# Optimization experiments

Hardware: AMD Instinct MI355X
Metric: run time of the kernel (lower is better)

## Reference

```python
import jax, jax.numpy as jnp
import numpy as np

B, N_ATOM, N_TOK = 1, 1536, 384
C_ATOM, C_PAIR, C_TOK = 128, 16, 384
C_HID, H, L = 32, 4, 3
HID = 2 * C_ATOM  # n_transition = 2
N_QUERY, N_KEY, INF = 32, 128, 1e9


def _ln(x, gamma=None, beta=None, eps=1e-5):
    mu = jnp.mean(x, axis=-1, keepdims=True)
    var = jnp.mean(jnp.square(x - mu), axis=-1, keepdims=True)
    y = (x - mu) * jax.lax.rsqrt(var + eps)
    if gamma is not None:
        y = y * gamma
    if beta is not None:
        y = y + beta
    return y


def _adaln(a, s, gamma_s, Wg, bg, Ws):
    an = _ln(a)            # LN without affine
    sn = _ln(s, gamma_s)   # scale-only LN
    return jax.nn.sigmoid(sn @ Wg + bg) * an + sn @ Ws


def _block_mask():
    # AtomTransformer.forward: 32-query x 128-key block-local mask
    offset = N_QUERY // 2 - 0.5
    n_center = N_ATOM // N_QUERY + 1
    centers = offset + jnp.arange(n_center, dtype=jnp.float32) * N_QUERY
    idx = jnp.arange(N_ATOM, dtype=jnp.float32)[:, None]
    row = (jnp.abs(idx - centers[None, :]) < N_QUERY / 2).astype(jnp.float32)
    col = (jnp.abs(idx - centers[None, :]) < N_KEY / 2).astype(jnp.float32)
    return (row @ col.T - 1.0) * INF   # [N,N]: 0 in-window, -INF outside


def _forward(ref_pos, ref_mask, ref_element, ref_charge, ref_atom_name_chars,
             ref_space_uid, token_mask, atom_to_token_index,
             W_feats, W_ref_offset, W_inv_sq, W_valid, W_l, W_m,
             W_mlp1, W_mlp2, W_mlp3, W_out_tok,
             attn_ada_gamma_s, attn_ada_Wg, attn_ada_bg, attn_ada_Ws,
             Wq, bq, Wk, Wv, lnz_g, lnz_b, Wb, Wgate, Wo, Wsg, bsg,
             tr_ada_gamma_s, tr_ada_Wg, tr_ada_bg, tr_ada_Ws,
             tr_W1, tr_W2, tr_Wog, tr_bog, tr_Wout):
    # --- RefAtomFeatureEmbedder (AF3 Alg 5 lines 1-6) ---
    feats = jnp.concatenate([
        ref_pos, ref_mask[..., None], ref_element, ref_charge[..., None],
        ref_atom_name_chars.reshape(B, N_ATOM, -1), ref_space_uid[..., None]], axis=-1)
    cl = feats @ W_feats                                     # [B,N,C_ATOM]
    d = ref_pos[:, None, :, :] - ref_pos[:, :, None, :]      # d[l,m] = pos[m]-pos[l]
    v = (ref_space_uid[:, None, :] == ref_space_uid[:, :, None]).astype(jnp.float32)[..., None]
    plm = (d @ W_ref_offset) * v
    inv_sq = 1.0 / (1.0 + jnp.sum(d * d, axis=-1, keepdims=True))
    plm = plm + (inv_sq @ W_inv_sq) * v + (v @ W_valid) * v  # [B,N,N,C_PAIR]
    ql = cl
    # --- single -> pair conditioning + pair MLP ---
    crelu = jax.nn.relu(cl)
    plm = plm + (crelu @ W_l)[:, :, None, :] + (crelu @ W_m)[:, None, :, :]
    h = jax.nn.relu(plm) @ W_mlp1
    h = jax.nn.relu(h) @ W_mlp2
    h = jax.nn.relu(h) @ W_mlp3
    plm = plm + h
    # --- AtomTransformer (Alg 7) -> DiffusionTransformer (Alg 23) ---
    beta = _block_mask()                                     # [N,N]
    atom_mask = jnp.einsum('blt,bt->bl', atom_to_token_index, token_mask)
    mask_bias = (atom_mask - 1.0)[:, None, None, :] * INF    # [B,1,1,N]
    a, s = ql, cl
    inv_sqrt = 1.0 / np.sqrt(C_HID)
    for i in range(L):
        # AttentionPairBias (Alg 24)
        an = _adaln(a, s, attn_ada_gamma_s[i], attn_ada_Wg[i], attn_ada_bg[i], attn_ada_Ws[i])
        q = (an @ Wq[i] + bq[i]).reshape(B, N_ATOM, H, C_HID)
        k = (an @ Wk[i]).reshape(B, N_ATOM, H, C_HID)
        vv = (an @ Wv[i]).reshape(B, N_ATOM, H, C_HID)
        zb = _ln(plm, lnz_g[i], lnz_b[i]) @ Wb[i]            # [B,N,N,H]
        logits = (jnp.einsum('bqhc,bkhc->bhqk', q, k) * inv_sqrt
                  + jnp.moveaxis(zb, -1, 1) + beta[None, None] + mask_bias)
        A = jax.nn.softmax(logits, axis=-1)
        o = jnp.einsum('bhqk,bkhc->bqhc', A, vv)
        g = jax.nn.sigmoid(an @ Wgate[i]).reshape(B, N_ATOM, H, C_HID)
        o = (g * o).reshape(B, N_ATOM, H * C_HID) @ Wo[i]
        attn_out = jax.nn.sigmoid(s @ Wsg[i] + bsg[i]) * o
        # ConditionedTransitionBlock (Alg 25) on pre-attention a (Alg 23)
        tn = _adaln(a, s, tr_ada_gamma_s[i], tr_ada_Wg[i], tr_ada_bg[i], tr_ada_Ws[i])
        hh = jax.nn.silu(tn @ tr_W1[i]) * (tn @ tr_W2[i])
        tr_out = jax.nn.sigmoid(s @ tr_Wog[i] + tr_bog[i]) * (hh @ tr_Wout[i])
        a = attn_out + tr_out
    # --- mean-aggregate atoms -> tokens (Alg 5 line 15) ---
    al = jax.nn.relu(a @ W_out_tok)                          # [B,N,C_TOK]
    counts = jnp.maximum(jnp.sum(atom_to_token_index, axis=1), 1.0)
    a_tok = jnp.einsum('blt,blc->btc', atom_to_token_index, al) / counts[..., None]
    return a_tok


def setup_inputs() -> dict:
    key = jax.random.key(0)
    ks = iter(jax.random.split(key, 80))

    def nrm(shape, scale=0.02):
        return jax.random.normal(next(ks), shape, dtype=jnp.float32) * scale

    inp = {}
    inp['ref_pos'] = jax.random.normal(next(ks), (B, N_ATOM, 3), dtype=jnp.float32) * 3.0
    inp['ref_mask'] = jnp.ones((B, N_ATOM), jnp.float32)
    elem = jax.random.randint(next(ks), (B, N_ATOM), 0, 128)
    inp['ref_element'] = jax.nn.one_hot(elem, 128, dtype=jnp.float32)
    inp['ref_charge'] = jax.random.normal(next(ks), (B, N_ATOM), dtype=jnp.float32)
    chars = jax.random.randint(next(ks), (B, N_ATOM, 4), 0, 64)
    inp['ref_atom_name_chars'] = jax.nn.one_hot(chars, 64, dtype=jnp.float32)
    inp['ref_space_uid'] = jnp.broadcast_to(
        (jnp.arange(N_ATOM) // 8).astype(jnp.float32), (B, N_ATOM))
    inp['token_mask'] = jnp.ones((B, N_TOK), jnp.float32)
    tok = (jnp.arange(N_ATOM) * N_TOK) // N_ATOM  # ~4 atoms per token
    inp['atom_to_token_index'] = jnp.broadcast_to(
        jax.nn.one_hot(tok, N_TOK, dtype=jnp.float32), (B, N_ATOM, N_TOK))
    # embedder params
    inp['W_feats'] = nrm((390, C_ATOM))
    inp['W_ref_offset'] = nrm((3, C_PAIR))
    inp['W_inv_sq'] = nrm((1, C_PAIR))
    inp['W_valid'] = nrm((1, C_PAIR))
    inp['W_l'] = nrm((C_ATOM, C_PAIR))
    inp['W_m'] = nrm((C_ATOM, C_PAIR))
    inp['W_mlp1'] = nrm((C_PAIR, C_PAIR))
    inp['W_mlp2'] = nrm((C_PAIR, C_PAIR))
    inp['W_mlp3'] = nrm((C_PAIR, C_PAIR))
    inp['W_out_tok'] = nrm((C_ATOM, C_TOK))
    # DiffusionTransformer params, stacked over L blocks
    inp['attn_ada_gamma_s'] = jnp.ones((L, C_ATOM), jnp.float32)
    inp['attn_ada_Wg'] = nrm((L, C_ATOM, C_ATOM))
    inp['attn_ada_bg'] = jnp.zeros((L, C_ATOM), jnp.float32)
    inp['attn_ada_Ws'] = nrm((L, C_ATOM, C_ATOM))
    inp['Wq'] = nrm((L, C_ATOM, H * C_HID))
    inp['bq'] = jnp.zeros((L, H * C_HID), jnp.float32)
    inp['Wk'] = nrm((L, C_ATOM, H * C_HID))
    inp['Wv'] = nrm((L, C_ATOM, H * C_HID))
    inp['lnz_g'] = jnp.ones((L, C_PAIR), jnp.float32)
    inp['lnz_b'] = jnp.zeros((L, C_PAIR), jnp.float32)
    inp['Wb'] = nrm((L, C_PAIR, H))
    inp['Wgate'] = nrm((L, C_ATOM, H * C_HID))
    inp['Wo'] = nrm((L, H * C_HID, C_ATOM))
    inp['Wsg'] = nrm((L, C_ATOM, C_ATOM))
    inp['bsg'] = jnp.full((L, C_ATOM), -2.0, jnp.float32)
    inp['tr_ada_gamma_s'] = jnp.ones((L, C_ATOM), jnp.float32)
    inp['tr_ada_Wg'] = nrm((L, C_ATOM, C_ATOM))
    inp['tr_ada_bg'] = jnp.zeros((L, C_ATOM), jnp.float32)
    inp['tr_ada_Ws'] = nrm((L, C_ATOM, C_ATOM))
    inp['tr_W1'] = nrm((L, C_ATOM, HID))
    inp['tr_W2'] = nrm((L, C_ATOM, HID))
    inp['tr_Wog'] = nrm((L, C_ATOM, C_ATOM))
    inp['tr_bog'] = jnp.full((L, C_ATOM), -2.0, jnp.float32)
    inp['tr_Wout'] = nrm((L, HID, C_ATOM))
    return inp


def reference(ref_pos, ref_mask, ref_element, ref_charge, ref_atom_name_chars,
              ref_space_uid, token_mask, atom_to_token_index,
              W_feats, W_ref_offset, W_inv_sq, W_valid, W_l, W_m,
              W_mlp1, W_mlp2, W_mlp3, W_out_tok,
              attn_ada_gamma_s, attn_ada_Wg, attn_ada_bg, attn_ada_Ws,
              Wq, bq, Wk, Wv, lnz_g, lnz_b, Wb, Wgate, Wo, Wsg, bsg,
              tr_ada_gamma_s, tr_ada_Wg, tr_ada_bg, tr_ada_Ws,
              tr_W1, tr_W2, tr_Wog, tr_bog, tr_Wout):
    return _forward(ref_pos, ref_mask, ref_element, ref_charge, ref_atom_name_chars,
                    ref_space_uid, token_mask, atom_to_token_index,
                    W_feats, W_ref_offset, W_inv_sq, W_valid, W_l, W_m,
                    W_mlp1, W_mlp2, W_mlp3, W_out_tok,
                    attn_ada_gamma_s, attn_ada_Wg, attn_ada_bg, attn_ada_Ws,
                    Wq, bq, Wk, Wv, lnz_g, lnz_b, Wb, Wgate, Wo, Wsg, bsg,
                    tr_ada_gamma_s, tr_ada_Wg, tr_ada_bg, tr_ada_Ws,
                    tr_W1, tr_W2, tr_Wog, tr_bog, tr_Wout)
```

## Files before the change

kernel.cpp:

```cpp
#include <hip/hip_runtime.h>
#include <math.h>

#define N_ATOM 1536
#define NB     48
#define NLAYER 3
#define NC     196608L
#define ZSTRIDE 786432L

struct GD { const float* A; const float* B; float* C; const float* ks; const float* bias;
            int act; int ldb; int ldc; int _pad; };
struct GB { GD g[18]; };

__global__ __launch_bounds__(128) void embed_tok_kernel(
    const float* __restrict__ pos, const float* __restrict__ rmask,
    const float* __restrict__ elem, const float* __restrict__ charge,
    const float* __restrict__ chars, const float* __restrict__ uid,
    const float* __restrict__ Wf, const float* __restrict__ W_l, const float* __restrict__ W_m,
    const float* __restrict__ a2t, const float* __restrict__ tmask,
    float* __restrict__ cl, float* __restrict__ aa, float* __restrict__ clnorm,
    float* __restrict__ pl, float* __restrict__ pm,
    int* __restrict__ tok, float* __restrict__ counts, float* __restrict__ amask)
{
  int l = blockIdx.x, c = threadIdx.x;
  __shared__ int sidx[6];
  __shared__ float red[128];
  __shared__ float crow[128];
  if (elem[(long)l * 128 + c] > 0.5f) sidx[0] = c;
  float v0 = chars[(long)l * 256 + c];
  if (v0 > 0.5f) sidx[1 + (c >> 6)] = c & 63;
  float v1 = chars[(long)l * 256 + 128 + c];
  if (v1 > 0.5f) sidx[3 + (c >> 6)] = c & 63;
  for (int j = c; j < 384; j += 128)
    if (a2t[(long)l * 384 + j] > 0.5f) sidx[5] = j;
  __syncthreads();
  float acc = pos[l * 3 + 0] * Wf[c]
            + pos[l * 3 + 1] * Wf[128 + c]
            + pos[l * 3 + 2] * Wf[256 + c]
            + rmask[l] * Wf[384 + c]
            + Wf[(4 + sidx[0]) * 128 + c]
            + charge[l] * Wf[132 * 128 + c]
            + Wf[(133 + sidx[1]) * 128 + c]
            + Wf[(197 + sidx[2]) * 128 + c]
            + Wf[(261 + sidx[3]) * 128 + c]
            + Wf[(325 + sidx[4]) * 128 + c]
            + uid[l] * Wf[389 * 128 + c];
  long gi = (long)l * 128 + c;
  cl[gi] = acc; aa[gi] = acc; crow[c] = fmaxf(acc, 0.f);
  red[c] = acc; __syncthreads();
  for (int s = 64; s > 0; s >>= 1) { if (c < s) red[c] += red[c + s]; __syncthreads(); }
  float mu = red[0] * (1.f / 128.f); __syncthreads();
  float d = acc - mu; red[c] = d * d; __syncthreads();
  for (int s = 64; s > 0; s >>= 1) { if (c < s) red[c] += red[c + s]; __syncthreads(); }
  clnorm[gi] = d * rsqrtf(red[0] * (1.f / 128.f) + 1e-5f);
  if (c < 32) {
    const float* W = (c < 16) ? W_l : W_m;
    int o = c & 15;
    float s = 0.f;
    for (int cc = 0; cc < 128; cc++) s = fmaf(crow[cc], W[cc * 16 + o], s);
    if (c < 16) pl[l * 16 + o] = s; else pm[l * 16 + o] = s;
  }
  if (c == 127) {
    int j = sidx[5];
    tok[l] = j; amask[l] = tmask[j];
    atomicAdd(counts + j, 1.0f);
  }
}

__global__ __launch_bounds__(128) void adaln_kernel(
    const float* __restrict__ a,
    const float* __restrict__ sgA, const float* __restrict__ adA,
    const float* __restrict__ sgT, const float* __restrict__ adT,
    float* __restrict__ an, float* __restrict__ tn)
{
  __shared__ float red[128];
  int l = blockIdx.x, c = threadIdx.x;
  float x = a[(long)l * 128 + c];
  red[c] = x; __syncthreads();
  for (int s = 64; s > 0; s >>= 1) { if (c < s) red[c] += red[c + s]; __syncthreads(); }
  float mu = red[0] * (1.f / 128.f); __syncthreads();
  float d = x - mu; red[c] = d * d; __syncthreads();
  for (int s = 64; s > 0; s >>= 1) { if (c < s) red[c] += red[c + s]; __syncthreads(); }
  float nv = d * rsqrtf(red[0] * (1.f / 128.f) + 1e-5f);
  long i = (long)l * 128 + c;
  an[i] = sgA[i] * nv + adA[i];
  tn[i] = sgT[i] * nv + adT[i];
}

__device__ __forceinline__ void gemm64_body(float* sm, const float* A, const float* B, float* C,
                                            const float* ks, const float* bias, int act,
                                            int ldb, int ldc, int row0, int col0) {
  float* As = sm; float* Bs = sm + 2176;
  int tid = threadIdx.x;
  int tx = tid & 15, ty = tid >> 4;
  float acc[4][4] = {};
  for (int k0 = 0; k0 < 128; k0 += 32) {
    __syncthreads();
    { int r = tid >> 3, k4 = tid & 7;
#pragma unroll
      for (int half = 0; half < 2; half++) {
        int row = r + half * 32;
        float4 v = *(const float4*)(A + (long)(row0 + row) * 128 + k0 + k4 * 4);
        if (ks) { const float* kp = ks + k0 + k4 * 4; v.x *= kp[0]; v.y *= kp[1]; v.z *= kp[2]; v.w *= kp[3]; }
        As[(k4 * 4 + 0) * 68 + row] = v.x; As[(k4 * 4 + 1) * 68 + row] = v.y;
        As[(k4 * 4 + 2) * 68 + row] = v.z; As[(k4 * 4 + 3) * 68 + row] = v.w;
      } }
    { int kk = tid >> 4, n4 = tid & 15;
#pragma unroll
      for (int half = 0; half < 2; half++) {
        int k = kk + half * 16;
        *(float4*)&Bs[k * 68 + n4 * 4] = *(const float4*)(B + (long)(k0 + k) * ldb + col0 + n4 * 4);
      } }
    __syncthreads();
#pragma unroll
    for (int kk = 0; kk < 32; kk++) {
      float4 a = *(const float4*)&As[kk * 68 + ty * 4];
      float4 b = *(const float4*)&Bs[kk * 68 + tx * 4];
      float av[4] = {a.x, a.y, a.z, a.w}, bv[4] = {b.x, b.y, b.z, b.w};
#pragma unroll
      for (int i = 0; i < 4; i++)
#pragma unroll
        for (int j = 0; j < 4; j++) acc[i][j] = fmaf(av[i], bv[j], acc[i][j]);
    }
  }
  __syncthreads();
#pragma unroll
  for (int i = 0; i < 4; i++) {
    int row = row0 + ty * 4 + i;
#pragma unroll
    for (int j = 0; j < 4; j++) {
      int col = col0 + tx * 4 + j;
      float x = acc[i][j];
      if (bias) x += bias[col];
      if (act == 1) x = 1.f / (1.f + expf(-x));
      else if (act == 2) x = fmaxf(x, 0.f);
      C[(long)row * ldc + col] = x;
    }
  }
}

__global__ __launch_bounds__(256) void gemm64(GB args, int M)
{
  __shared__ float sm[4352];
  GD d = args.g[blockIdx.z];
  gemm64_body(sm, d.A, d.B, d.C, d.ks, d.bias, d.act, d.ldb, d.ldc, blockIdx.y * 64, blockIdx.x * 64);
}

__global__ __launch_bounds__(256) void zpre_kernel(
    const float* __restrict__ pos, const float* __restrict__ uid,
    const float* __restrict__ Wro, const float* __restrict__ Winv, const float* __restrict__ Wval,
    const float* __restrict__ M1, const float* __restrict__ M2, const float* __restrict__ M3,
    const float* __restrict__ Lg, const float* __restrict__ Lb, const float* __restrict__ Wb,
    const float* __restrict__ pl, const float* __restrict__ pm, float* __restrict__ zb,
    GB ba)
{
  __shared__ float sm[4352];
  int bid = blockIdx.x, tid = threadIdx.x;
  if (bid >= 768) {
    int u = bid - 768;
    GD d = ba.g[u / 48];
    int tt = u % 48;
    gemm64_body(sm, d.A, d.B, d.C, d.ks, d.bias, d.act, d.ldb, d.ldc, (tt >> 1) * 64, (tt & 1) * 64);
    return;
  }
  if (tid < 48)  sm[tid] = Wro[tid];
  if (tid < 16)  { sm[48 + tid] = Winv[tid]; sm[64 + tid] = Wval[tid]; }
  sm[80 + tid] = M1[tid]; sm[336 + tid] = M2[tid]; sm[592 + tid] = M3[tid];
  if (tid < 48)  { sm[848 + tid] = Lg[tid]; sm[896 + tid] = Lb[tid]; }
  if (tid < 192) sm[944 + tid] = Wb[tid];
  __syncthreads();
  const float* sWro = sm;      const float* sWinv = sm + 48;  const float* sWval = sm + 64;
  const float* sM1 = sm + 80;  const float* sM2 = sm + 336;   const float* sM3 = sm + 592;
  const float* sLg = sm + 848; const float* sLb = sm + 896;   const float* sWb = sm + 944;
  int b = bid >> 4;
  int pc = (bid & 15) * 256 + tid;
  int qi = pc >> 7, kj = pc & 127;
  int l = b * 32 + qi, m = b * 32 - 48 + kj;
  long base = ((long)(b * 32 + qi) * 128 + kj) * 4;
  if (m < 0 || m >= N_ATOM) {
    for (int i = 0; i < NLAYER; i++)
      for (int h = 0; h < 4; h++) zb[i * ZSTRIDE + base + h] = 0.f;
    return;
  }
  float dx = pos[m * 3 + 0] - pos[l * 3 + 0];
  float dy = pos[m * 3 + 1] - pos[l * 3 + 1];
  float dz = pos[m * 3 + 2] - pos[l * 3 + 2];
  float v = (uid[m] == uid[l]) ? 1.f : 0.f;
  float inv = 1.f / (1.f + dx * dx + dy * dy + dz * dz);
  float pv[16], ha[16], hb[16];
#pragma unroll
  for (int j = 0; j < 16; j++)
    pv[j] = v * (dx * sWro[j] + dy * sWro[16 + j] + dz * sWro[32 + j] + inv * sWinv[j] + sWval[j])
            + pl[l * 16 + j] + pm[m * 16 + j];
#pragma unroll
  for (int jo = 0; jo < 16; jo++) { float s = 0.f; for (int ji = 0; ji < 16; ji++) s = fmaf(fmaxf(pv[ji], 0.f), sM1[ji * 16 + jo], s); ha[jo] = s; }
#pragma unroll
  for (int jo = 0; jo < 16; jo++) { float s = 0.f; for (int ji = 0; ji < 16; ji++) s = fmaf(fmaxf(ha[ji], 0.f), sM2[ji * 16 + jo], s); hb[jo] = s; }
#pragma unroll
  for (int jo = 0; jo < 16; jo++) { float s = 0.f; for (int ji = 0; ji < 16; ji++) s = fmaf(fmaxf(hb[ji], 0.f), sM3[ji * 16 + jo], s); ha[jo] = s; }
#pragma unroll
  for (int j = 0; j < 16; j++) pv[j] += ha[j];
  for (int i = 0; i < NLAYER; i++) {
    float mu = 0.f;
#pragma unroll
    for (int j = 0; j < 16; j++) mu += pv[j];
    mu *= (1.f / 16.f);
    float var = 0.f;
#pragma unroll
    for (int j = 0; j < 16; j++) { float dd = pv[j] - mu; var += dd * dd; }
    var *= (1.f / 16.f);
    float rs = rsqrtf(var + 1e-5f);
    float zn[16];
#pragma unroll
    for (int j = 0; j < 16; j++) zn[j] = (pv[j] - mu) * rs * sLg[i * 16 + j] + sLb[i * 16 + j];
    for (int h = 0; h < 4; h++) {
      float s = 0.f;
#pragma unroll
      for (int j = 0; j < 16; j++) s = fmaf(zn[j], sWb[i * 64 + j * 4 + h], s);
      zb[i * ZSTRIDE + base + h] = s;
    }
  }
}

__global__ __launch_bounds__(256) void attn_kernel(
    const float* __restrict__ qb, const float* __restrict__ kb, const float* __restrict__ vb,
    const float* __restrict__ gb, const float* __restrict__ zb, const float* __restrict__ amask,
    float* __restrict__ go)
{
  __shared__ float qs[32][36], ks[128][36], vs[128][36], ps[32][132];
  __shared__ float red[32][8];
  int b = blockIdx.x, h = blockIdx.y, t = threadIdx.x;
  int kbase = b * 32 - 48;
  {
    int qi = t >> 3, c4 = t & 7;
    *(float4*)&qs[qi][c4 * 4] = *(const float4*)(qb + (long)(b * 32 + qi) * 128 + h * 32 + c4 * 4);
  }
  for (int idx = t; idx < 128 * 8; idx += 256) {
    int kj = idx >> 3, c4 = idx & 7;
    int m = kbase + kj;
    float4 kv = make_float4(0.f, 0.f, 0.f, 0.f), vv = make_float4(0.f, 0.f, 0.f, 0.f);
    if (m >= 0 && m < N_ATOM) {
      kv = *(const float4*)(kb + (long)m * 128 + h * 32 + c4 * 4);
      vv = *(const float4*)(vb + (long)m * 128 + h * 32 + c4 * 4);
    }
    *(float4*)&ks[kj][c4 * 4] = kv;
    *(float4*)&vs[kj][c4 * 4] = vv;
  }
  __syncthreads();
  const float isq = 0.17677669529663687f;
  for (int p = t; p < 4096; p += 256) {
    int qi = p >> 7, kj = p & 127;
    int m = kbase + kj;
    float s = 0.f;
#pragma unroll
    for (int c4 = 0; c4 < 8; c4++) {
      float4 a = *(const float4*)&qs[qi][c4 * 4];
      float4 k4 = *(const float4*)&ks[kj][c4 * 4];
      s = fmaf(a.x, k4.x, s); s = fmaf(a.y, k4.y, s);
      s = fmaf(a.z, k4.z, s); s = fmaf(a.w, k4.w, s);
    }
    float logit;
    if (m >= 0 && m < N_ATOM) {
      logit = s * isq + zb[(((long)(b * 32 + qi)) * 128 + kj) * 4 + h] + (amask[m] - 1.f) * 1e9f;
    } else {
      logit = -1e9f;
    }
    ps[qi][kj] = logit;
  }
  __syncthreads();
  int row = t >> 3, ln8 = t & 7;
  float mx = -1e30f;
  for (int kj = ln8; kj < 128; kj += 8) mx = fmaxf(mx, ps[row][kj]);
  red[row][ln8] = mx; __syncthreads();
  if (ln8 == 0) {
    float m2 = red[row][0];
#pragma unroll
    for (int j = 1; j < 8; j++) m2 = fmaxf(m2, red[row][j]);
    red[row][0] = m2;
  }
  __syncthreads();
  mx = red[row][0];
  float sm = 0.f;
  for (int kj = ln8; kj < 128; kj += 8) { float e = expf(ps[row][kj] - mx); ps[row][kj] = e; sm += e; }
  __syncthreads();
  red[row][ln8] = sm; __syncthreads();
  if (ln8 == 0) {
    float s2 = 0.f;
#pragma unroll
    for (int j = 0; j < 8; j++) s2 += red[row][j];
    red[row][0] = 1.f / s2;
  }
  __syncthreads();
  float r = red[row][0];
  for (int kj = ln8; kj < 128; kj += 8) ps[row][kj] *= r;
  __syncthreads();
  {
    int qi = t >> 3, c4 = t & 7;
    float4 acc = make_float4(0.f, 0.f, 0.f, 0.f);
#pragma unroll 4
    for (int kj = 0; kj < 128; kj++) {
      float p = ps[qi][kj];
      float4 v = *(const float4*)&vs[kj][c4 * 4];
      acc.x = fmaf(p, v.x, acc.x); acc.y = fmaf(p, v.y, acc.y);
      acc.z = fmaf(p, v.z, acc.z); acc.w = fmaf(p, v.w, acc.w);
    }
    long gi = (long)(b * 32 + qi) * 128 + h * 32 + c4 * 4;
    float4 g = *(const float4*)(gb + gi);
    acc.x *= g.x; acc.y *= g.y; acc.z *= g.z; acc.w *= g.w;
    *(float4*)(go + gi) = acc;
  }
}

__global__ __launch_bounds__(256) void gemm_dual32(
    const float* __restrict__ A1, const float* __restrict__ B1,
    const float* __restrict__ h1, const float* __restrict__ h2, const float* __restrict__ B2,
    const float* __restrict__ g1, const float* __restrict__ g2,
    float* __restrict__ C)
{
  __shared__ float As[32 * 36];
  __shared__ float Bs[32 * 68];
  const int N = 128;
  int t = threadIdx.x;
  int row0 = blockIdx.y * 32, col0 = blockIdx.x * 64;
  int tx = t & 15, ty = t >> 4;
  float acc1[2][4] = {}, acc2[2][4] = {};
  for (int k0 = 0; k0 < 128; k0 += 32) {
    __syncthreads();
    { int r = t >> 3, k4 = t & 7;
      float4 v = *(const float4*)(A1 + (long)(row0 + r) * 128 + k0 + k4 * 4);
      As[(k4 * 4 + 0) * 36 + r] = v.x; As[(k4 * 4 + 1) * 36 + r] = v.y;
      As[(k4 * 4 + 2) * 36 + r] = v.z; As[(k4 * 4 + 3) * 36 + r] = v.w;
    }
    for (int e = t; e < 512; e += 256) {
      int k = e >> 4, n4 = e & 15;
      *(float4*)&Bs[k * 68 + n4 * 4] = *(const float4*)(B1 + (long)(k0 + k) * N + col0 + n4 * 4);
    }
    __syncthreads();
#pragma unroll
    for (int kk = 0; kk < 32; kk++) {
      float a0 = As[kk * 36 + ty * 2], a1 = As[kk * 36 + ty * 2 + 1];
      float4 b = *(const float4*)&Bs[kk * 68 + tx * 4];
      float bv[4] = {b.x, b.y, b.z, b.w};
#pragma unroll
      for (int j = 0; j < 4; j++) {
        acc1[0][j] = fmaf(a0, bv[j], acc1[0][j]);
        acc1[1][j] = fmaf(a1, bv[j], acc1[1][j]);
      }
    }
  }
  for (int k0 = 0; k0 < 256; k0 += 32) {
    __syncthreads();
    { int r = t >> 3, k4 = t & 7;
      long o = (long)(row0 + r) * 256 + k0 + k4 * 4;
      float4 x = *(const float4*)(h1 + o);
      float4 y = *(const float4*)(h2 + o);
      As[(k4 * 4 + 0) * 36 + r] = (x.x / (1.f + expf(-x.x))) * y.x;
      As[(k4 * 4 + 1) * 36 + r] = (x.y / (1.f + expf(-x.y))) * y.y;
      As[(k4 * 4 + 2) * 36 + r] = (x.z / (1.f + expf(-x.z))) * y.z;
      As[(k4 * 4 + 3) * 36 + r] = (x.w / (1.f + expf(-x.w))) * y.w;
    }
    for (int e = t; e < 512; e += 256) {
      int k = e >> 4, n4 = e & 15;
      *(float4*)&Bs[k * 68 + n4 * 4] = *(const float4*)(B2 + (long)(k0 + k) * N + col0 + n4 * 4);
    }
    __syncthreads();
#pragma unroll
    for (int kk = 0; kk < 32; kk++) {
      float a0 = As[kk * 36 + ty * 2], a1 = As[kk * 36 + ty * 2 + 1];
      float4 b = *(const float4*)&Bs[kk * 68 + tx * 4];
      float bv[4] = {b.x, b.y, b.z, b.w};
#pragma unroll
      for (int j = 0; j < 4; j++) {
        acc2[0][j] = fmaf(a0, bv[j], acc2[0][j]);
        acc2[1][j] = fmaf(a1, bv[j], acc2[1][j]);
      }
    }
  }
#pragma unroll
  for (int i = 0; i < 2; i++) {
    long o = (long)(row0 + ty * 2 + i) * N + col0 + tx * 4;
    float4 ga = *(const float4*)(g1 + o);
    float4 gb = *(const float4*)(g2 + o);
    float4 r;
    r.x = ga.x * acc1[i][0] + gb.x * acc2[i][0];
    r.y = ga.y * acc1[i][1] + gb.y * acc2[i][1];
    r.z = ga.z * acc1[i][2] + gb.z * acc2[i][2];
    r.w = ga.w * acc1[i][3] + gb.w * acc2[i][3];
    *(float4*)(C + o) = r;
  }
}

__global__ __launch_bounds__(256) void gemm_scatter(
    const float* __restrict__ A, const float* __restrict__ B,
    const int* __restrict__ tok, const float* __restrict__ counts,
    float* __restrict__ out, int K)
{
  __shared__ float As[32][68];
  __shared__ float Bs[32][68];
  int tid = threadIdx.x;
  int row0 = blockIdx.y * 64, col0 = blockIdx.x * 64;
  int tx = tid & 15, ty = tid >> 4;
  float acc[4][4] = {};
  for (int k0 = 0; k0 < K; k0 += 32) {
    __syncthreads();
    { int r = tid >> 3, k4 = tid & 7;
#pragma unroll
      for (int half = 0; half < 2; half++) {
        int row = r + half * 32;
        float4 v = *(const float4*)(A + (long)(row0 + row) * K + k0 + k4 * 4);
        As[k4 * 4 + 0][row] = v.x; As[k4 * 4 + 1][row] = v.y;
        As[k4 * 4 + 2][row] = v.z; As[k4 * 4 + 3][row] = v.w;
      } }
    { int kk = tid >> 4, n4 = tid & 15;
#pragma unroll
      for (int half = 0; half < 2; half++) {
        int k = kk + half * 16;
        float4 v = *(const float4*)(B + (long)(k0 + k) * 384 + col0 + n4 * 4);
        *(float4*)&Bs[k][n4 * 4] = v;
      } }
    __syncthreads();
#pragma unroll
    for (int kk = 0; kk < 32; kk++) {
      float4 a = *(const float4*)&As[kk][ty * 4];
      float4 b = *(const float4*)&Bs[kk][tx * 4];
      float av[4] = {a.x, a.y, a.z, a.w}, bv[4] = {b.x, b.y, b.z, b.w};
#pragma unroll
      for (int i = 0; i < 4; i++)
#pragma unroll
        for (int j = 0; j < 4; j++) acc[i][j] = fmaf(av[i], bv[j], acc[i][j]);
    }
  }
  __syncthreads();
#pragma unroll
  for (int i = 0; i < 4; i++) {
    int row = row0 + ty * 4 + i;
    int tk = tok[row];
    float inv = 1.f / fmaxf(counts[tk], 1.f);
#pragma unroll
    for (int j = 0; j < 4; j++) {
      int col = col0 + tx * 4 + j;
      atomicAdd(&out[(long)tk * 384 + col], fmaxf(acc[i][j], 0.f) * inv);
    }
  }
}

extern "C" void kernel_launch(void* const* d_in, const int* in_sizes, int n_in,
                              void* d_out, int out_size, void* d_ws, size_t ws_size,
                              hipStream_t stream)
{
  const float* pos    = (const float*)d_in[0];
  const float* rmask  = (const float*)d_in[1];
  const float* elem   = (const float*)d_in[2];
  const float* charge = (const float*)d_in[3];
  const float* chars  = (const float*)d_in[4];
  const float* uid    = (const float*)d_in[5];
  const float* tmask  = (const float*)d_in[6];
  const float* a2t    = (const float*)d_in[7];
  const float* Wf     = (const float*)d_in[8];
  const float* Wro    = (const float*)d_in[9];
  const float* Winv   = (const float*)d_in[10];
  const float* Wval   = (const float*)d_in[11];
  const float* W_l    = (const float*)d_in[12];
  const float* W_m    = (const float*)d_in[13];
  const float* M1     = (const float*)d_in[14];
  const float* M2     = (const float*)d_in[15];
  const float* M3     = (const float*)d_in[16];
  const float* Wtok   = (const float*)d_in[17];
  const float* gA     = (const float*)d_in[18];
  const float* WgA    = (const float*)d_in[19];
  const float* bgA    = (const float*)d_in[20];
  const float* WsA    = (const float*)d_in[21];
  const float* Wq     = (const float*)d_in[22];
  const float* bq     = (const float*)d_in[23];
  const float* Wk     = (const float*)d_in[24];
  const float* Wv     = (const float*)d_in[25];
  const float* Lg     = (const float*)d_in[26];
  const float* Lb     = (const float*)d_in[27];
  const float* Wb     = (const float*)d_in[28];
  const float* Wgate  = (const float*)d_in[29];
  const float* Wo     = (const float*)d_in[30];
  const float* Wsg    = (const float*)d_in[31];
  const float* bsg    = (const float*)d_in[32];
  const float* gT     = (const float*)d_in[33];
  const float* WgT    = (const float*)d_in[34];
  const float* bgT    = (const float*)d_in[35];
  const float* WsT    = (const float*)d_in[36];
  const float* trW1   = (const float*)d_in[37];
  const float* trW2   = (const float*)d_in[38];
  const float* Wog    = (const float*)d_in[39];
  const float* bog    = (const float*)d_in[40];
  const float* Wout   = (const float*)d_in[41];
  float* out = (float*)d_out;

  float* ws = (float*)d_ws;
  size_t off = 0;
  auto alloc = [&](size_t n) { float* p = ws + off; off += n; return p; };
  float* cl     = alloc(NC);
  float* aa     = alloc(NC);
  float* clnorm = alloc(NC);
  float* an     = alloc(NC);
  float* tn     = alloc(NC);
  float* qbuf   = alloc(NC);
  float* kbuf   = alloc(NC);
  float* vbuf   = alloc(NC);
  float* gbuf   = alloc(NC);
  float* gobuf  = alloc(NC);
  float* h1     = alloc((size_t)N_ATOM * 256);
  float* h2     = alloc((size_t)N_ATOM * 256);
  float* pl     = alloc((size_t)N_ATOM * 16);
  float* pm     = alloc((size_t)N_ATOM * 16);
  float* zbias  = alloc((size_t)NLAYER * ZSTRIDE);
  float* sgA    = alloc(NC * NLAYER);
  float* adA    = alloc(NC * NLAYER);
  float* sgT    = alloc(NC * NLAYER);
  float* adT    = alloc(NC * NLAYER);
  float* gsg    = alloc(NC * NLAYER);
  float* gog    = alloc(NC * NLAYER);
  float* counts = alloc(384);
  float* amask  = alloc(N_ATOM);
  int*   tok    = (int*)alloc(N_ATOM);
  (void)ws_size; (void)in_sizes; (void)n_in; (void)out_size;

  (void)hipMemsetAsync(counts, 0, 384 * sizeof(float), stream);
  (void)hipMemsetAsync(out, 0, (size_t)384 * 384 * sizeof(float), stream);

  embed_tok_kernel<<<N_ATOM, 128, 0, stream>>>(pos, rmask, elem, charge, chars, uid, Wf,
                                               W_l, W_m, a2t, tmask,
                                               cl, aa, clnorm, pl, pm, tok, counts, amask);

  {
    GB ba = {};
    for (int i = 0; i < NLAYER; i++) {
      size_t o = (size_t)i * NC;
      ba.g[i * 6 + 0] = { clnorm, WgA + i * 16384, sgA + o, gA + i * 128, bgA + i * 128, 1, 128, 128, 0 };
      ba.g[i * 6 + 1] = { clnorm, WsA + i * 16384, adA + o, gA + i * 128, nullptr,       0, 128, 128, 0 };
      ba.g[i * 6 + 2] = { clnorm, WgT + i * 16384, sgT + o, gT + i * 128, bgT + i * 128, 1, 128, 128, 0 };
      ba.g[i * 6 + 3] = { clnorm, WsT + i * 16384, adT + o, gT + i * 128, nullptr,       0, 128, 128, 0 };
      ba.g[i * 6 + 4] = { cl,     Wsg + i * 16384, gsg + o, nullptr,      bsg + i * 128, 1, 128, 128, 0 };
      ba.g[i * 6 + 5] = { cl,     Wog + i * 16384, gog + o, nullptr,      bog + i * 128, 1, 128, 128, 0 };
    }
    zpre_kernel<<<768 + 864, 256, 0, stream>>>(pos, uid, Wro, Winv, Wval, M1, M2, M3,
                                               Lg, Lb, Wb, pl, pm, zbias, ba);
  }

  for (int i = 0; i < NLAYER; i++) {
    size_t o = (size_t)i * NC;
    adaln_kernel<<<N_ATOM, 128, 0, stream>>>(aa, sgA + o, adA + o, sgT + o, adT + o, an, tn);
    {
      GB ba = {};
      ba.g[0] = { an, Wq + i * 16384,        qbuf, nullptr, bq + i * 128, 0, 128, 128, 0 };
      ba.g[1] = { an, Wk + i * 16384,        kbuf, nullptr, nullptr,      0, 128, 128, 0 };
      ba.g[2] = { an, Wv + i * 16384,        vbuf, nullptr, nullptr,      0, 128, 128, 0 };
      ba.g[3] = { an, Wgate + i * 16384,     gbuf, nullptr, nullptr,      1, 128, 128, 0 };
      ba.g[4] = { tn, trW1 + i * 32768,       h1,  nullptr, nullptr,      0, 256, 256, 0 };
      ba.g[5] = { tn, trW1 + i * 32768 + 128, h1 + 128, nullptr, nullptr, 0, 256, 256, 0 };
      ba.g[6] = { tn, trW2 + i * 32768,       h2,  nullptr, nullptr,      0, 256, 256, 0 };
      ba.g[7] = { tn, trW2 + i * 32768 + 128, h2 + 128, nullptr, nullptr, 0, 256, 256, 0 };
      gemm64<<<dim3(2, 24, 8), 256, 0, stream>>>(ba, N_ATOM);
    }
    attn_kernel<<<dim3(NB, 4), 256, 0, stream>>>(qbuf, kbuf, vbuf, gbuf,
                                                 zbias + (size_t)i * ZSTRIDE, amask, gobuf);
    gemm_dual32<<<dim3(2, 48), 256, 0, stream>>>(gobuf, Wo + i * 16384, h1, h2, Wout + i * 32768,
                                                 gsg + o, gog + o, aa);
  }

  gemm_scatter<<<dim3(6, 24), 256, 0, stream>>>(aa, Wtok, tok, counts, out, 128);
}
```

Before: 357.0 us.

## Fuse AdaLN into per-layer QKV/transition GEMM and precompute SwiGLU product

Removes the separate adaln kernel and its an/tn intermediate buffers. The per-layer projection GEMM now computes LayerNorm statistics and the AdaLN modulation on its A tile in shared memory. The transition blocks compute both W1 and W2 tiles at once and write silu(h1)*h2 into a single hh buffer, so gemm_dual32 reads half as much data. This cuts one launch and several global round-trips per layer, at the cost of recomputing LN per column tile and using more shared memory per block (about 52KB), which may lower occupancy.

```diff
diff --git a/kernel.cpp b/kernel.cpp
--- a/kernel.cpp
+++ b/kernel.cpp
@@ -66,26 +66,6 @@
   }
 }
 
-__global__ __launch_bounds__(128) void adaln_kernel(
-    const float* __restrict__ a,
-    const float* __restrict__ sgA, const float* __restrict__ adA,
-    const float* __restrict__ sgT, const float* __restrict__ adT,
-    float* __restrict__ an, float* __restrict__ tn)
-{
-  __shared__ float red[128];
-  int l = blockIdx.x, c = threadIdx.x;
-  float x = a[(long)l * 128 + c];
-  red[c] = x; __syncthreads();
-  for (int s = 64; s > 0; s >>= 1) { if (c < s) red[c] += red[c + s]; __syncthreads(); }
-  float mu = red[0] * (1.f / 128.f); __syncthreads();
-  float d = x - mu; red[c] = d * d; __syncthreads();
-  for (int s = 64; s > 0; s >>= 1) { if (c < s) red[c] += red[c + s]; __syncthreads(); }
-  float nv = d * rsqrtf(red[0] * (1.f / 128.f) + 1e-5f);
-  long i = (long)l * 128 + c;
-  an[i] = sgA[i] * nv + adA[i];
-  tn[i] = sgT[i] * nv + adT[i];
-}
-
 __device__ __forceinline__ void gemm64_body(float* sm, const float* A, const float* B, float* C,
                                             const float* ks, const float* bias, int act,
                                             int ldb, int ldc, int row0, int col0) {
@@ -136,13 +116,6 @@
       C[(long)row * ldc + col] = x;
     }
   }
-}
-
-__global__ __launch_bounds__(256) void gemm64(GB args, int M)
-{
-  __shared__ float sm[4352];
-  GD d = args.g[blockIdx.z];
-  gemm64_body(sm, d.A, d.B, d.C, d.ks, d.bias, d.act, d.ldb, d.ldc, blockIdx.y * 64, blockIdx.x * 64);
 }
 
 __global__ __launch_bounds__(256) void zpre_kernel(
@@ -221,6 +194,134 @@
   }
 }
 
+__global__ __launch_bounds__(256) void adaqkv_kernel(
+    const float* __restrict__ aa,
+    const float* __restrict__ sgA, const float* __restrict__ adA,
+    const float* __restrict__ sgT, const float* __restrict__ adT,
+    const float* __restrict__ Wq, const float* __restrict__ bq,
+    const float* __restrict__ Wk, const float* __restrict__ Wv, const float* __restrict__ Wgate,
+    const float* __restrict__ W1, const float* __restrict__ W2,
+    float* __restrict__ qbuf, float* __restrict__ kbuf, float* __restrict__ vbuf,
+    float* __restrict__ gbuf, float* __restrict__ hh)
+{
+  __shared__ float sm[13184];
+  float* mu = sm; float* rs = sm + 64;
+  float* Af = sm + 128; float* Bs = sm + 8832; float* B2s = sm + 11008;
+  int u = blockIdx.x, t = threadIdx.x;
+  bool tr = (u >= 192);
+  int rowt, colt;
+  const float *sg, *ad;
+  if (!tr) { int tt = u % 48; rowt = tt >> 1; colt = tt & 1; sg = sgA; ad = adA; }
+  else     { int u2 = u - 192; rowt = u2 >> 2; colt = u2 & 3; sg = sgT; ad = adT; }
+  int row0 = rowt * 64, col0 = colt * 64;
+
+  for (int e = t; e < 2048; e += 256) {
+    int row = e >> 5, k4 = e & 31;
+    float4 v = *(const float4*)(aa + (long)(row0 + row) * 128 + k4 * 4);
+    Af[(k4 * 4 + 0) * 68 + row] = v.x; Af[(k4 * 4 + 1) * 68 + row] = v.y;
+    Af[(k4 * 4 + 2) * 68 + row] = v.z; Af[(k4 * 4 + 3) * 68 + row] = v.w;
+  }
+  __syncthreads();
+  if (t < 64) {
+    float s = 0.f;
+    for (int k = 0; k < 128; k++) s += Af[k * 68 + t];
+    float m_ = s * (1.f / 128.f);
+    float v_ = 0.f;
+    for (int k = 0; k < 128; k++) { float d = Af[k * 68 + t] - m_; v_ += d * d; }
+    mu[t] = m_; rs[t] = rsqrtf(v_ * (1.f / 128.f) + 1e-5f);
+  }
+  __syncthreads();
+  for (int e = t; e < 2048; e += 256) {
+    int row = e >> 5, k4 = e & 31;
+    long go = (long)(row0 + row) * 128 + k4 * 4;
+    float4 sv = *(const float4*)(sg + go);
+    float4 av = *(const float4*)(ad + go);
+    float m_ = mu[row], r_ = rs[row];
+    Af[(k4 * 4 + 0) * 68 + row] = sv.x * ((Af[(k4 * 4 + 0) * 68 + row] - m_) * r_) + av.x;
+    Af[(k4 * 4 + 1) * 68 + row] = sv.y * ((Af[(k4 * 4 + 1) * 68 + row] - m_) * r_) + av.y;
+    Af[(k4 * 4 + 2) * 68 + row] = sv.z * ((Af[(k4 * 4 + 2) * 68 + row] - m_) * r_) + av.z;
+    Af[(k4 * 4 + 3) * 68 + row] = sv.w * ((Af[(k4 * 4 + 3) * 68 + row] - m_) * r_) + av.w;
+  }
+  int tx = t & 15, ty = t >> 4;
+  if (!tr) {
+    int m = u / 48;
+    const float* Bmat = (m == 0) ? Wq : (m == 1) ? Wk : (m == 2) ? Wv : Wgate;
+    float* C = (m == 0) ? qbuf : (m == 1) ? kbuf : (m == 2) ? vbuf : gbuf;
+    float acc[4][4] = {};
+    for (int k0 = 0; k0 < 128; k0 += 32) {
+      __syncthreads();
+      { int kk = t >> 4, n4 = t & 15;
+#pragma unroll
+        for (int half = 0; half < 2; half++) {
+          int k = kk + half * 16;
+          *(float4*)&Bs[k * 68 + n4 * 4] = *(const float4*)(Bmat + (long)(k0 + k) * 128 + col0 + n4 * 4);
+        } }
+      __syncthreads();
+#pragma unroll
+      for (int kk = 0; kk < 32; kk++) {
+        float4 a = *(const float4*)&Af[(k0 + kk) * 68 + ty * 4];
+        float4 b = *(const float4*)&Bs[kk * 68 + tx * 4];
+        float av[4] = {a.x, a.y, a.z, a.w}, bv[4] = {b.x, b.y, b.z, b.w};
+#pragma unroll
+        for (int i = 0; i < 4; i++)
+#pragma unroll
+          for (int j = 0; j < 4; j++) acc[i][j] = fmaf(av[i], bv[j], acc[i][j]);
+      }
+    }
+#pragma unroll
+    for (int i = 0; i < 4; i++) {
+      int row = row0 + ty * 4 + i;
+#pragma unroll
+      for (int j = 0; j < 4; j++) {
+        int col = col0 + tx * 4 + j;
+        float x = acc[i][j];
+        if (m == 0) x += bq[col];
+        if (m == 3) x = 1.f / (1.f + expf(-x));
+        C[(long)row * 128 + col] = x;
+      }
+    }
+  } else {
+    float acc1[4][4] = {}, acc2[4][4] = {};
+    for (int k0 = 0; k0 < 128; k0 += 32) {
+      __syncthreads();
+      { int kk = t >> 4, n4 = t & 15;
+#pragma unroll
+        for (int half = 0; half < 2; half++) {
+          int k = kk + half * 16;
+          *(float4*)&Bs[k * 68 + n4 * 4]  = *(const float4*)(W1 + (long)(k0 + k) * 256 + col0 + n4 * 4);
+          *(float4*)&B2s[k * 68 + n4 * 4] = *(const float4*)(W2 + (long)(k0 + k) * 256 + col0 + n4 * 4);
+        } }
+      __syncthreads();
+#pragma unroll
+      for (int kk = 0; kk < 32; kk++) {
+        float4 a = *(const float4*)&Af[(k0 + kk) * 68 + ty * 4];
+        float4 b = *(const float4*)&Bs[kk * 68 + tx * 4];
+        float4 c = *(const float4*)&B2s[kk * 68 + tx * 4];
+        float av[4] = {a.x, a.y, a.z, a.w};
+        float bv[4] = {b.x, b.y, b.z, b.w};
+        float cv[4] = {c.x, c.y, c.z, c.w};
+#pragma unroll
+        for (int i = 0; i < 4; i++)
+#pragma unroll
+          for (int j = 0; j < 4; j++) {
+            acc1[i][j] = fmaf(av[i], bv[j], acc1[i][j]);
+            acc2[i][j] = fmaf(av[i], cv[j], acc2[i][j]);
+          }
+      }
+    }
+#pragma unroll
+    for (int i = 0; i < 4; i++) {
+      int row = row0 + ty * 4 + i;
+#pragma unroll
+      for (int j = 0; j < 4; j++) {
+        int col = col0 + tx * 4 + j;
+        float x = acc1[i][j];
+        hh[(long)row * 256 + col] = (x / (1.f + expf(-x))) * acc2[i][j];
+      }
+    }
+  }
+}
+
 __global__ __launch_bounds__(256) void attn_kernel(
     const float* __restrict__ qb, const float* __restrict__ kb, const float* __restrict__ vb,
     const float* __restrict__ gb, const float* __restrict__ zb, const float* __restrict__ amask,
@@ -312,7 +413,7 @@
 
 __global__ __launch_bounds__(256) void gemm_dual32(
     const float* __restrict__ A1, const float* __restrict__ B1,
-    const float* __restrict__ h1, const float* __restrict__ h2, const float* __restrict__ B2,
+    const float* __restrict__ hh, const float* __restrict__ B2,
     const float* __restrict__ g1, const float* __restrict__ g2,
     float* __restrict__ C)
 {
@@ -350,13 +451,9 @@
   for (int k0 = 0; k0 < 256; k0 += 32) {
     __syncthreads();
     { int r = t >> 3, k4 = t & 7;
-      long o = (long)(row0 + r) * 256 + k0 + k4 * 4;
-      float4 x = *(const float4*)(h1 + o);
-      float4 y = *(const float4*)(h2 + o);
-      As[(k4 * 4 + 0) * 36 + r] = (x.x / (1.f + expf(-x.x))) * y.x;
-      As[(k4 * 4 + 1) * 36 + r] = (x.y / (1.f + expf(-x.y))) * y.y;
-      As[(k4 * 4 + 2) * 36 + r] = (x.z / (1.f + expf(-x.z))) * y.z;
-      As[(k4 * 4 + 3) * 36 + r] = (x.w / (1.f + expf(-x.w))) * y.w;
+      float4 v = *(const float4*)(hh + (long)(row0 + r) * 256 + k0 + k4 * 4);
+      As[(k4 * 4 + 0) * 36 + r] = v.x; As[(k4 * 4 + 1) * 36 + r] = v.y;
+      As[(k4 * 4 + 2) * 36 + r] = v.z; As[(k4 * 4 + 3) * 36 + r] = v.w;
     }
     for (int e = t; e < 512; e += 256) {
       int k = e >> 4, n4 = e & 15;
@@ -497,15 +594,12 @@
   float* cl     = alloc(NC);
   float* aa     = alloc(NC);
   float* clnorm = alloc(NC);
-  float* an     = alloc(NC);
-  float* tn     = alloc(NC);
   float* qbuf   = alloc(NC);
   float* kbuf   = alloc(NC);
   float* vbuf   = alloc(NC);
   float* gbuf   = alloc(NC);
   float* gobuf  = alloc(NC);
-  float* h1     = alloc((size_t)N_ATOM * 256);
-  float* h2     = alloc((size_t)N_ATOM * 256);
+  float* hh     = alloc((size_t)N_ATOM * 256);
   float* pl     = alloc((size_t)N_ATOM * 16);
   float* pm     = alloc((size_t)N_ATOM * 16);
   float* zbias  = alloc((size_t)NLAYER * ZSTRIDE);
@@ -544,22 +638,14 @@
 
   for (int i = 0; i < NLAYER; i++) {
     size_t o = (size_t)i * NC;
-    adaln_kernel<<<N_ATOM, 128, 0, stream>>>(aa, sgA + o, adA + o, sgT + o, adT + o, an, tn);
-    {
-      GB ba = {};
-      ba.g[0] = { an, Wq + i * 16384,        qbuf, nullptr, bq + i * 128, 0, 128, 128, 0 };
-      ba.g[1] = { an, Wk + i * 16384,        kbuf, nullptr, nullptr,      0, 128, 128, 0 };
-      ba.g[2] = { an, Wv + i * 16384,        vbuf, nullptr, nullptr,      0, 128, 128, 0 };
-      ba.g[3] = { an, Wgate + i * 16384,     gbuf, nullptr, nullptr,      1, 128, 128, 0 };
-      ba.g[4] = { tn, trW1 + i * 32768,       h1,  nullptr, nullptr,      0, 256, 256, 0 };
-      ba.g[5] = { tn, trW1 + i * 32768 + 128, h1 + 128, nullptr, nullptr, 0, 256, 256, 0 };
-      ba.g[6] = { tn, trW2 + i * 32768,       h2,  nullptr, nullptr,      0, 256, 256, 0 };
-      ba.g[7] = { tn, trW2 + i * 32768 + 128, h2 + 128, nullptr, nullptr, 0, 256, 256, 0 };
-      gemm64<<<dim3(2, 24, 8), 256, 0, stream>>>(ba, N_ATOM);
-    }
+    adaqkv_kernel<<<288, 256, 0, stream>>>(aa, sgA + o, adA + o, sgT + o, adT + o,
+                                           Wq + i * 16384, bq + i * 128,
+                                           Wk + i * 16384, Wv + i * 16384, Wgate + i * 16384,
+                                           trW1 + i * 32768, trW2 + i * 32768,
+                                           qbuf, kbuf, vbuf, gbuf, hh);
     attn_kernel<<<dim3(NB, 4), 256, 0, stream>>>(qbuf, kbuf, vbuf, gbuf,
                                                  zbias + (size_t)i * ZSTRIDE, amask, gobuf);
-    gemm_dual32<<<dim3(2, 48), 256, 0, stream>>>(gobuf, Wo + i * 16384, h1, h2, Wout + i * 32768,
+    gemm_dual32<<<dim3(2, 48), 256, 0, stream>>>(gobuf, Wo + i * 16384, hh, Wout + i * 32768,
                                                  gsg + o, gog + o, aa);
   }
 
```

Result: slower. 380.1 us (+6.5%).

## Split attention blocks into 16-query halves with shuffle-based softmax and split-K PV

Applied to the files above, without the earlier changes.

Each attention block now handles 16 queries instead of 32, doubling the grid to 96x4 blocks so more CUs are busy. Softmax reductions use wavefront shuffles over 16 lanes instead of shared-memory reductions with several barriers. The PV product splits the key range across two thread halves and combines them with a shuffle. The cost is that K/V tiles are loaded twice per query block.

```diff
diff --git a/kernel.cpp b/kernel.cpp
--- a/kernel.cpp
+++ b/kernel.cpp
@@ -226,13 +226,14 @@
     const float* __restrict__ gb, const float* __restrict__ zb, const float* __restrict__ amask,
     float* __restrict__ go)
 {
-  __shared__ float qs[32][36], ks[128][36], vs[128][36], ps[32][132];
-  __shared__ float red[32][8];
-  int b = blockIdx.x, h = blockIdx.y, t = threadIdx.x;
+  __shared__ float qs[16][36], ks[128][36], vs[128][36], ps[16][132];
+  int bx = blockIdx.x, h = blockIdx.y, t = threadIdx.x;
+  int b = bx >> 1, half = bx & 1;
+  int q0 = b * 32 + half * 16;
   int kbase = b * 32 - 48;
-  {
+  if (t < 128) {
     int qi = t >> 3, c4 = t & 7;
-    *(float4*)&qs[qi][c4 * 4] = *(const float4*)(qb + (long)(b * 32 + qi) * 128 + h * 32 + c4 * 4);
+    *(float4*)&qs[qi][c4 * 4] = *(const float4*)(qb + (long)(q0 + qi) * 128 + h * 32 + c4 * 4);
   }
   for (int idx = t; idx < 128 * 8; idx += 256) {
     int kj = idx >> 3, c4 = idx & 7;
@@ -247,7 +248,7 @@
   }
   __syncthreads();
   const float isq = 0.17677669529663687f;
-  for (int p = t; p < 4096; p += 256) {
+  for (int p = t; p < 2048; p += 256) {
     int qi = p >> 7, kj = p & 127;
     int m = kbase + kj;
     float s = 0.f;
@@ -260,53 +261,48 @@
     }
     float logit;
     if (m >= 0 && m < N_ATOM) {
-      logit = s * isq + zb[(((long)(b * 32 + qi)) * 128 + kj) * 4 + h] + (amask[m] - 1.f) * 1e9f;
+      logit = s * isq + zb[(((long)(q0 + qi)) * 128 + kj) * 4 + h] + (amask[m] - 1.f) * 1e9f;
     } else {
       logit = -1e9f;
     }
     ps[qi][kj] = logit;
   }
   __syncthreads();
-  int row = t >> 3, ln8 = t & 7;
-  float mx = -1e30f;
-  for (int kj = ln8; kj < 128; kj += 8) mx = fmaxf(mx, ps[row][kj]);
-  red[row][ln8] = mx; __syncthreads();
-  if (ln8 == 0) {
-    float m2 = red[row][0];
-#pragma unroll
-    for (int j = 1; j < 8; j++) m2 = fmaxf(m2, red[row][j]);
-    red[row][0] = m2;
-  }
-  __syncthreads();
-  mx = red[row][0];
-  float sm = 0.f;
-  for (int kj = ln8; kj < 128; kj += 8) { float e = expf(ps[row][kj] - mx); ps[row][kj] = e; sm += e; }
-  __syncthreads();
-  red[row][ln8] = sm; __syncthreads();
-  if (ln8 == 0) {
-    float s2 = 0.f;
-#pragma unroll
-    for (int j = 0; j < 8; j++) s2 += red[row][j];
-    red[row][0] = 1.f / s2;
-  }
-  __syncthreads();
-  float r = red[row][0];
-  for (int kj = ln8; kj < 128; kj += 8) ps[row][kj] *= r;
-  __syncthreads();
   {
-    int qi = t >> 3, c4 = t & 7;
+    int row = t >> 4, ln = t & 15;
+    float mx = -1e30f;
+    for (int kj = ln; kj < 128; kj += 16) mx = fmaxf(mx, ps[row][kj]);
+#pragma unroll
+    for (int o = 8; o > 0; o >>= 1) mx = fmaxf(mx, __shfl_xor(mx, o));
+    float sm = 0.f;
+    for (int kj = ln; kj < 128; kj += 16) { float e = expf(ps[row][kj] - mx); ps[row][kj] = e; sm += e; }
+#pragma unroll
+    for (int o = 8; o > 0; o >>= 1) sm += __shfl_xor(sm, o);
+    float r = 1.f / sm;
+    for (int kj = ln; kj < 128; kj += 16) ps[row][kj] *= r;
+  }
+  __syncthreads();
+  {
+    int qi = t >> 4, seg = (t >> 3) & 1, c4 = t & 7;
     float4 acc = make_float4(0.f, 0.f, 0.f, 0.f);
+    int kj0 = seg * 64;
 #pragma unroll 4
-    for (int kj = 0; kj < 128; kj++) {
+    for (int kj = kj0; kj < kj0 + 64; kj++) {
       float p = ps[qi][kj];
       float4 v = *(const float4*)&vs[kj][c4 * 4];
       acc.x = fmaf(p, v.x, acc.x); acc.y = fmaf(p, v.y, acc.y);
       acc.z = fmaf(p, v.z, acc.z); acc.w = fmaf(p, v.w, acc.w);
     }
-    long gi = (long)(b * 32 + qi) * 128 + h * 32 + c4 * 4;
-    float4 g = *(const float4*)(gb + gi);
-    acc.x *= g.x; acc.y *= g.y; acc.z *= g.z; acc.w *= g.w;
-    *(float4*)(go + gi) = acc;
+    acc.x += __shfl_xor(acc.x, 8);
+    acc.y += __shfl_xor(acc.y, 8);
+    acc.z += __shfl_xor(acc.z, 8);
+    acc.w += __shfl_xor(acc.w, 8);
+    if (seg == 0) {
+      long gi = (long)(q0 + qi) * 128 + h * 32 + c4 * 4;
+      float4 g = *(const float4*)(gb + gi);
+      acc.x *= g.x; acc.y *= g.y; acc.z *= g.z; acc.w *= g.w;
+      *(float4*)(go + gi) = acc;
+    }
   }
 }
 
@@ -557,7 +553,7 @@
       ba.g[7] = { tn, trW2 + i * 32768 + 128, h2 + 128, nullptr, nullptr, 0, 256, 256, 0 };
       gemm64<<<dim3(2, 24, 8), 256, 0, stream>>>(ba, N_ATOM);
     }
-    attn_kernel<<<dim3(NB, 4), 256, 0, stream>>>(qbuf, kbuf, vbuf, gbuf,
+    attn_kernel<<<dim3(96, 4), 256, 0, stream>>>(qbuf, kbuf, vbuf, gbuf,
                                                  zbias + (size_t)i * ZSTRIDE, amask, gobuf);
     gemm_dual32<<<dim3(2, 48), 256, 0, stream>>>(gobuf, Wo + i * 16384, h1, h2, Wout + i * 32768,
                                                  gsg + o, gog + o, aa);
```

New measurement: 351.5 us. No clear change (-1.5%).
